# Kernel tuning notes

Measured on AMD Instinct MI355X. Metric: run time of the kernel, lower is better.

The kernel has to match this reference:

```python
import jax, jax.numpy as jnp
import numpy as np

NUM_USERS = 50000
NUM_ITEMS = 100000
N = NUM_USERS + NUM_ITEMS
D = 64
K = 3
E = 1000000


def setup_inputs() -> dict:
    key = jax.random.key(0)
    k1, k2, k3, k4 = jax.random.split(key, 4)
    users_emb = jax.random.normal(k1, (NUM_USERS, D), dtype=jnp.float32)
    items_emb = jax.random.normal(k2, (NUM_ITEMS, D), dtype=jnp.float32)
    src = jax.random.randint(k3, (E,), 0, N, dtype=jnp.int32)
    dst = jax.random.randint(k4, (E,), 0, N, dtype=jnp.int32)
    return {"users_emb": users_emb, "items_emb": items_emb, "src": src, "dst": dst}


def reference(users_emb, items_emb, src, dst):
    all_emb = jnp.concatenate([users_emb, items_emb], axis=0)  # [N, D]
    # out_degrees: number of outgoing edges per node, clamped to >= 1
    deg = jax.ops.segment_sum(jnp.ones((E,), dtype=jnp.float32), src, num_segments=N)
    normed_deg = jnp.power(jnp.clip(deg, 1.0, None), -0.5)[:, None]  # [N, 1]

    def conv(emb):
        h = emb * normed_deg                                  # D^{-1/2} * x
        agg = jax.ops.segment_sum(h[src], dst, num_segments=N)  # copy_u + sum
        return agg * normed_deg                               # * D^{-1/2}

    acc = all_emb
    emb = all_emb
    for _ in range(K):
        emb = conv(emb)
        acc = acc + emb
    final = acc / (K + 1)  # mean over layer embeddings
    return final[:NUM_USERS], final[NUM_USERS:]
```

## Files before the change

### kernel.cpp

```cpp
#include <hip/hip_runtime.h>

#define NUSERS 50000
#define NITEMS 100000
#define NNODES 150000
#define DIM 64
#define BSTRIDE 32

static __device__ __forceinline__ float bf2f(unsigned short u) {
    return __uint_as_float(((unsigned)u) << 16);
}
static __device__ __forceinline__ unsigned short f2bf(float f) {
    unsigned u = __float_as_uint(f);
    return (unsigned short)((u + 0x7fffu + ((u >> 16) & 1u)) >> 16);
}
static __device__ __forceinline__ float4 cvt4(ushort4 u) {
    return make_float4(bf2f(u.x), bf2f(u.y), bf2f(u.z), bf2f(u.w));
}

__global__ void hist_place_kernel(const int4* __restrict__ src4,
                                  const int4* __restrict__ dst4,
                                  int* __restrict__ outdeg,
                                  int* __restrict__ indeg,
                                  int* __restrict__ csr, int E4) {
    int i = blockIdx.x * blockDim.x + threadIdx.x;
    if (i >= E4) return;
    int4 s = src4[i];
    int4 d = dst4[i];
    atomicAdd(&outdeg[s.x], 1);
    atomicAdd(&outdeg[s.y], 1);
    atomicAdd(&outdeg[s.z], 1);
    atomicAdd(&outdeg[s.w], 1);
    int r0 = atomicAdd(&indeg[d.x], 1);
    int r1 = atomicAdd(&indeg[d.y], 1);
    int r2 = atomicAdd(&indeg[d.z], 1);
    int r3 = atomicAdd(&indeg[d.w], 1);
    if (r0 < BSTRIDE) csr[d.x * BSTRIDE + r0] = s.x;
    if (r1 < BSTRIDE) csr[d.y * BSTRIDE + r1] = s.y;
    if (r2 < BSTRIDE) csr[d.z * BSTRIDE + r2] = s.z;
    if (r3 < BSTRIDE) csr[d.w * BSTRIDE + r3] = s.w;
}

__global__ void norm_kernel(const int* __restrict__ outdeg, float* __restrict__ norm) {
    int v = blockIdx.x * blockDim.x + threadIdx.x;
    if (v < NNODES) {
        float d = fmaxf((float)outdeg[v], 1.0f);
        norm[v] = rsqrtf(d);
    }
}

template <int FIRST, int LAST>
__global__ void gather_kernel(const int* __restrict__ csr,
                              const int* __restrict__ indeg,
                              const float* __restrict__ norm,
                              const ushort4* __restrict__ cur,
                              const float4* __restrict__ users4,
                              const float4* __restrict__ items4,
                              const ushort4* __restrict__ nxt0,
                              const ushort4* __restrict__ nxt1,
                              ushort4* __restrict__ out_bf,
                              float4* __restrict__ out_f32) {
    int t = blockIdx.x * blockDim.x + threadIdx.x;
    int v = t >> 4;
    int l = t & 15;
    if (v >= NNODES) return;
    int start = v * BSTRIDE;
    int cnt   = min(indeg[v], BSTRIDE);
    float4 sum = make_float4(0.f, 0.f, 0.f, 0.f);
#pragma unroll 4
    for (int k = 0; k < cnt; ++k) {
        int s = csr[start + k];
        float ns = norm[s];
        float4 r;
        if (FIRST) {
            r = (s < NUSERS) ? users4[s * 16 + l] : items4[(s - NUSERS) * 16 + l];
        } else {
            r = cvt4(cur[s * 16 + l]);
        }
        sum.x = fmaf(r.x, ns, sum.x);
        sum.y = fmaf(r.y, ns, sum.y);
        sum.z = fmaf(r.z, ns, sum.z);
        sum.w = fmaf(r.w, ns, sum.w);
    }
    float nv = norm[v];
    float4 val = make_float4(sum.x * nv, sum.y * nv, sum.z * nv, sum.w * nv);
    int o = v * 16 + l;
    if (!LAST) {
        out_bf[o] = make_ushort4(f2bf(val.x), f2bf(val.y), f2bf(val.z), f2bf(val.w));
    } else {
        float4 orig = (v < NUSERS) ? users4[o] : items4[(v - NUSERS) * 16 + l];
        float4 a0 = cvt4(nxt0[o]);
        float4 a1 = cvt4(nxt1[o]);
        float4 r;
        r.x = (orig.x + a0.x + a1.x + val.x) * 0.25f;
        r.y = (orig.y + a0.y + a1.y + val.y) * 0.25f;
        r.z = (orig.z + a0.z + a1.z + val.z) * 0.25f;
        r.w = (orig.w + a0.w + a1.w + val.w) * 0.25f;
        out_f32[o] = r;
    }
}

extern "C" void kernel_launch(void* const* d_in, const int* in_sizes, int n_in,
                              void* d_out, int out_size, void* d_ws, size_t ws_size,
                              hipStream_t stream) {
    const int* src = (const int*)d_in[2];
    const int* dst = (const int*)d_in[3];
    const int  E   = in_sizes[2];
    const float4* users4 = (const float4*)d_in[0];
    const float4* items4 = (const float4*)d_in[1];
    float4* out4 = (float4*)d_out;

    char* w = (char*)d_ws;
    int*   outdeg = (int*)w;      w += sizeof(int) * NNODES;
    int*   indeg  = (int*)w;      w += sizeof(int) * NNODES;
    float* norm   = (float*)w;    w += sizeof(float) * NNODES;
    int*   csr    = (int*)w;      w += sizeof(int) * (size_t)NNODES * BSTRIDE;
    ushort4* emb_a = (ushort4*)w; w += sizeof(unsigned short) * (size_t)NNODES * DIM;
    ushort4* emb_b = (ushort4*)w;

    const int BLK  = 256;
    const int gnod = (NNODES + BLK - 1) / BLK;
    const int E4   = E / 4;
    const int ghst = (E4 + BLK - 1) / BLK;
    const int ggat = (NNODES * 16 + BLK - 1) / BLK;

    hipMemsetAsync(outdeg, 0, sizeof(int) * NNODES * 2, stream);
    hist_place_kernel<<<ghst, BLK, 0, stream>>>((const int4*)src, (const int4*)dst,
                                                outdeg, indeg, csr, E4);
    norm_kernel<<<gnod, BLK, 0, stream>>>(outdeg, norm);

    gather_kernel<1, 0><<<ggat, BLK, 0, stream>>>(csr, indeg, norm,
                                                  (const ushort4*)nullptr, users4, items4,
                                                  nullptr, nullptr, emb_a, nullptr);
    gather_kernel<0, 0><<<ggat, BLK, 0, stream>>>(csr, indeg, norm,
                                                  emb_a, users4, items4,
                                                  nullptr, nullptr, emb_b, nullptr);
    gather_kernel<0, 1><<<ggat, BLK, 0, stream>>>(csr, indeg, norm,
                                                  emb_b, users4, items4,
                                                  emb_a, emb_b, nullptr, out4);
}
```

Baseline: 250.7 us.

## Carry pre-scaled embeddings so gathers skip per-edge norm lookups

Stores embeddings pre-multiplied by D^{-1/2}. The per-edge loop then only loads bf16 rows and adds them, and each node applies a single 1/deg factor. A prescale pass converts the fp32 inputs to scaled bf16, so the first layer gathers 128-byte rows instead of 256-byte fp32 rows. The final layer rescales the intermediates by sqrt(d). The histogram kernel also drops int4 vectorization in favour of one edge per thread. The trade-off is an extra pass over all nodes and possible bf16 precision drift from the rescaling.

```diff
diff --git a/kernel.cpp b/kernel.cpp
--- a/kernel.cpp
+++ b/kernel.cpp
@@ -16,87 +16,95 @@
 static __device__ __forceinline__ float4 cvt4(ushort4 u) {
     return make_float4(bf2f(u.x), bf2f(u.y), bf2f(u.z), bf2f(u.w));
 }
+static __device__ __forceinline__ ushort4 pack4(float4 v) {
+    return make_ushort4(f2bf(v.x), f2bf(v.y), f2bf(v.z), f2bf(v.w));
+}
 
-__global__ void hist_place_kernel(const int4* __restrict__ src4,
-                                  const int4* __restrict__ dst4,
+__global__ void hist_place_kernel(const int* __restrict__ src,
+                                  const int* __restrict__ dst,
                                   int* __restrict__ outdeg,
                                   int* __restrict__ indeg,
-                                  int* __restrict__ csr, int E4) {
-    int i = blockIdx.x * blockDim.x + threadIdx.x;
-    if (i >= E4) return;
-    int4 s = src4[i];
-    int4 d = dst4[i];
-    atomicAdd(&outdeg[s.x], 1);
-    atomicAdd(&outdeg[s.y], 1);
-    atomicAdd(&outdeg[s.z], 1);
-    atomicAdd(&outdeg[s.w], 1);
-    int r0 = atomicAdd(&indeg[d.x], 1);
-    int r1 = atomicAdd(&indeg[d.y], 1);
-    int r2 = atomicAdd(&indeg[d.z], 1);
-    int r3 = atomicAdd(&indeg[d.w], 1);
-    if (r0 < BSTRIDE) csr[d.x * BSTRIDE + r0] = s.x;
-    if (r1 < BSTRIDE) csr[d.y * BSTRIDE + r1] = s.y;
-    if (r2 < BSTRIDE) csr[d.z * BSTRIDE + r2] = s.z;
-    if (r3 < BSTRIDE) csr[d.w * BSTRIDE + r3] = s.w;
+                                  int* __restrict__ csr, int E) {
+    int e = blockIdx.x * blockDim.x + threadIdx.x;
+    if (e >= E) return;
+    int s = src[e];
+    int d = dst[e];
+    atomicAdd(&outdeg[s], 1);
+    int r = atomicAdd(&indeg[d], 1);
+    if (r < BSTRIDE) csr[d * BSTRIDE + r] = s;
 }
 
-__global__ void norm_kernel(const int* __restrict__ outdeg, float* __restrict__ norm) {
-    int v = blockIdx.x * blockDim.x + threadIdx.x;
-    if (v < NNODES) {
-        float d = fmaxf((float)outdeg[v], 1.0f);
-        norm[v] = rsqrtf(d);
-    }
+__global__ void prescale_kernel(const float4* __restrict__ users4,
+                                const float4* __restrict__ items4,
+                                const int* __restrict__ outdeg,
+                                ushort4* __restrict__ s0) {
+    int t = blockIdx.x * blockDim.x + threadIdx.x;
+    int v = t >> 4;
+    int l = t & 15;
+    if (v >= NNODES) return;
+    float ns = rsqrtf(fmaxf((float)outdeg[v], 1.0f));
+    float4 r = (v < NUSERS) ? users4[v * 16 + l] : items4[(v - NUSERS) * 16 + l];
+    r.x *= ns; r.y *= ns; r.z *= ns; r.w *= ns;
+    s0[v * 16 + l] = pack4(r);
 }
 
-template <int FIRST, int LAST>
-__global__ void gather_kernel(const int* __restrict__ csr,
-                              const int* __restrict__ indeg,
-                              const float* __restrict__ norm,
-                              const ushort4* __restrict__ cur,
-                              const float4* __restrict__ users4,
-                              const float4* __restrict__ items4,
-                              const ushort4* __restrict__ nxt0,
-                              const ushort4* __restrict__ nxt1,
-                              ushort4* __restrict__ out_bf,
-                              float4* __restrict__ out_f32) {
+__global__ void gather_mid_kernel(const int* __restrict__ csr,
+                                  const int* __restrict__ indeg,
+                                  const int* __restrict__ outdeg,
+                                  const ushort4* __restrict__ cur,
+                                  ushort4* __restrict__ nxt) {
     int t = blockIdx.x * blockDim.x + threadIdx.x;
     int v = t >> 4;
     int l = t & 15;
     if (v >= NNODES) return;
     int start = v * BSTRIDE;
-    int cnt   = min(indeg[v], BSTRIDE);
+    int cnt = min(indeg[v], BSTRIDE);
     float4 sum = make_float4(0.f, 0.f, 0.f, 0.f);
 #pragma unroll 4
     for (int k = 0; k < cnt; ++k) {
         int s = csr[start + k];
-        float ns = norm[s];
-        float4 r;
-        if (FIRST) {
-            r = (s < NUSERS) ? users4[s * 16 + l] : items4[(s - NUSERS) * 16 + l];
-        } else {
-            r = cvt4(cur[s * 16 + l]);
-        }
-        sum.x = fmaf(r.x, ns, sum.x);
-        sum.y = fmaf(r.y, ns, sum.y);
-        sum.z = fmaf(r.z, ns, sum.z);
-        sum.w = fmaf(r.w, ns, sum.w);
+        float4 r = cvt4(cur[s * 16 + l]);
+        sum.x += r.x; sum.y += r.y; sum.z += r.z; sum.w += r.w;
     }
-    float nv = norm[v];
-    float4 val = make_float4(sum.x * nv, sum.y * nv, sum.z * nv, sum.w * nv);
+    float inv_d = 1.0f / fmaxf((float)outdeg[v], 1.0f);
+    sum.x *= inv_d; sum.y *= inv_d; sum.z *= inv_d; sum.w *= inv_d;
+    nxt[v * 16 + l] = pack4(sum);
+}
+
+__global__ void gather_last_kernel(const int* __restrict__ csr,
+                                   const int* __restrict__ indeg,
+                                   const int* __restrict__ outdeg,
+                                   const ushort4* __restrict__ s2,
+                                   const ushort4* __restrict__ s1,
+                                   const float4* __restrict__ users4,
+                                   const float4* __restrict__ items4,
+                                   float4* __restrict__ out4) {
+    int t = blockIdx.x * blockDim.x + threadIdx.x;
+    int v = t >> 4;
+    int l = t & 15;
+    if (v >= NNODES) return;
+    int start = v * BSTRIDE;
+    int cnt = min(indeg[v], BSTRIDE);
+    float4 sum = make_float4(0.f, 0.f, 0.f, 0.f);
+#pragma unroll 4
+    for (int k = 0; k < cnt; ++k) {
+        int s = csr[start + k];
+        float4 r = cvt4(s2[s * 16 + l]);
+        sum.x += r.x; sum.y += r.y; sum.z += r.z; sum.w += r.w;
+    }
+    float d  = fmaxf((float)outdeg[v], 1.0f);
+    float ns = rsqrtf(d);
+    float sq = d * ns;
     int o = v * 16 + l;
-    if (!LAST) {
-        out_bf[o] = make_ushort4(f2bf(val.x), f2bf(val.y), f2bf(val.z), f2bf(val.w));
-    } else {
-        float4 orig = (v < NUSERS) ? users4[o] : items4[(v - NUSERS) * 16 + l];
-        float4 a0 = cvt4(nxt0[o]);
-        float4 a1 = cvt4(nxt1[o]);
-        float4 r;
-        r.x = (orig.x + a0.x + a1.x + val.x) * 0.25f;
-        r.y = (orig.y + a0.y + a1.y + val.y) * 0.25f;
-        r.z = (orig.z + a0.z + a1.z + val.z) * 0.25f;
-        r.w = (orig.w + a0.w + a1.w + val.w) * 0.25f;
-        out_f32[o] = r;
-    }
+    float4 orig = (v < NUSERS) ? users4[o] : items4[(v - NUSERS) * 16 + l];
+    float4 a1 = cvt4(s1[o]);
+    float4 a2 = cvt4(s2[o]);
+    float4 r;
+    r.x = (orig.x + (a1.x + a2.x) * sq + sum.x * ns) * 0.25f;
+    r.y = (orig.y + (a1.y + a2.y) * sq + sum.y * ns) * 0.25f;
+    r.z = (orig.z + (a1.z + a2.z) * sq + sum.z * ns) * 0.25f;
+    r.w = (orig.w + (a1.w + a2.w) * sq + sum.w * ns) * 0.25f;
+    out4[o] = r;
 }
 
 extern "C" void kernel_launch(void* const* d_in, const int* in_sizes, int n_in,
@@ -110,31 +118,23 @@
     float4* out4 = (float4*)d_out;
 
     char* w = (char*)d_ws;
-    int*   outdeg = (int*)w;      w += sizeof(int) * NNODES;
-    int*   indeg  = (int*)w;      w += sizeof(int) * NNODES;
-    float* norm   = (float*)w;    w += sizeof(float) * NNODES;
-    int*   csr    = (int*)w;      w += sizeof(int) * (size_t)NNODES * BSTRIDE;
-    ushort4* emb_a = (ushort4*)w; w += sizeof(unsigned short) * (size_t)NNODES * DIM;
-    ushort4* emb_b = (ushort4*)w;
+    int*     outdeg = (int*)w;    w += sizeof(int) * NNODES;
+    int*     indeg  = (int*)w;    w += sizeof(int) * NNODES;
+    int*     csr    = (int*)w;    w += sizeof(int) * (size_t)NNODES * BSTRIDE;
+    ushort4* s0     = (ushort4*)w; w += sizeof(unsigned short) * (size_t)NNODES * DIM;
+    ushort4* s1     = (ushort4*)w; w += sizeof(unsigned short) * (size_t)NNODES * DIM;
+    ushort4* s2     = (ushort4*)w;
 
     const int BLK  = 256;
-    const int gnod = (NNODES + BLK - 1) / BLK;
-    const int E4   = E / 4;
-    const int ghst = (E4 + BLK - 1) / BLK;
+    const int gedg = (E + BLK - 1) / BLK;
     const int ggat = (NNODES * 16 + BLK - 1) / BLK;
 
     hipMemsetAsync(outdeg, 0, sizeof(int) * NNODES * 2, stream);
-    hist_place_kernel<<<ghst, BLK, 0, stream>>>((const int4*)src, (const int4*)dst,
-                                                outdeg, indeg, csr, E4);
-    norm_kernel<<<gnod, BLK, 0, stream>>>(outdeg, norm);
+    hist_place_kernel<<<gedg, BLK, 0, stream>>>(src, dst, outdeg, indeg, csr, E);
+    prescale_kernel<<<ggat, BLK, 0, stream>>>(users4, items4, outdeg, s0);
 
-    gather_kernel<1, 0><<<ggat, BLK, 0, stream>>>(csr, indeg, norm,
-                                                  (const ushort4*)nullptr, users4, items4,
-                                                  nullptr, nullptr, emb_a, nullptr);
-    gather_kernel<0, 0><<<ggat, BLK, 0, stream>>>(csr, indeg, norm,
-                                                  emb_a, users4, items4,
-                                                  nullptr, nullptr, emb_b, nullptr);
-    gather_kernel<0, 1><<<ggat, BLK, 0, stream>>>(csr, indeg, norm,
-                                                  emb_b, users4, items4,
-                                                  emb_a, emb_b, nullptr, out4);
+    gather_mid_kernel<<<ggat, BLK, 0, stream>>>(csr, indeg, outdeg, s0, s1);
+    gather_mid_kernel<<<ggat, BLK, 0, stream>>>(csr, indeg, outdeg, s1, s2);
+    gather_last_kernel<<<ggat, BLK, 0, stream>>>(csr, indeg, outdeg, s2, s1,
+                                                 users4, items4, out4);
 }
```

Result: faster. 213.1 us (-15.0%).
